# Kernel tuning notes

Measured on AMD Instinct MI355X. Metric: run time of the kernel, lower is better.

Reference implementation:

```python
import jax, jax.numpy as jnp
import numpy as np

N_NODES = 100000   # total nodes in batched graph
N_EDGES = 800000   # total edges
N_GRAPH = 64       # graphs in batch
N_PASSES = 3


def _mlp(x, w1, b1, w2, b2, w3, b3):
    h = jax.nn.relu(x @ w1 + b1)
    h = jax.nn.relu(h @ w2 + b2)
    return h @ w3 + b3


def _segment_mean(x, ids, num_segments):
    # tf.math.unsorted_segment_mean: empty segments -> 0
    s = jax.ops.segment_sum(x, ids, num_segments=num_segments)
    c = jax.ops.segment_sum(jnp.ones((x.shape[0], 1), x.dtype), ids, num_segments=num_segments)
    return s / jnp.maximum(c, 1.0)


def setup_inputs() -> dict:
    key = jax.random.key(0)
    ks = jax.random.split(key, 16)
    nodes = jax.random.normal(ks[0], (N_NODES, 32), jnp.float32)
    edges = jax.random.normal(ks[1], (N_EDGES, 32), jnp.float32)
    globals_ = jax.random.normal(ks[2], (N_GRAPH, 16), jnp.float32)
    senders = jax.random.randint(ks[3], (N_EDGES,), 0, N_NODES, jnp.int32)
    receivers = jax.random.randint(ks[4], (N_EDGES,), 0, N_NODES, jnp.int32)
    node_gid = jnp.sort(jax.random.randint(ks[5], (N_NODES,), 0, N_GRAPH, jnp.int32))
    edge_gid = jnp.sort(jax.random.randint(ks[6], (N_EDGES,), 0, N_GRAPH, jnp.int32))

    def dense(k, din, dout):
        kw, _ = jax.random.split(k)
        w = jax.random.normal(kw, (din, dout), jnp.float32) / np.sqrt(din).astype(np.float32)
        b = jnp.zeros((dout,), jnp.float32)
        return w, b

    e_w1, e_b1 = dense(ks[7], 112, 16)
    e_w2, e_b2 = dense(ks[8], 16, 16)
    e_w3, e_b3 = dense(ks[9], 16, 32)
    n_w1, n_b1 = dense(ks[10], 80, 16)
    n_w2, n_b2 = dense(ks[11], 16, 16)
    n_w3, n_b3 = dense(ks[12], 16, 32)
    g_w1, g_b1 = dense(ks[13], 80, 16)
    g_w2, g_b2 = dense(ks[14], 16, 16)
    g_w3, g_b3 = dense(ks[15], 16, 16)
    return dict(nodes=nodes, edges=edges, globals_=globals_, senders=senders,
                receivers=receivers, node_gid=node_gid, edge_gid=edge_gid,
                e_w1=e_w1, e_b1=e_b1, e_w2=e_w2, e_b2=e_b2, e_w3=e_w3, e_b3=e_b3,
                n_w1=n_w1, n_b1=n_b1, n_w2=n_w2, n_b2=n_b2, n_w3=n_w3, n_b3=n_b3,
                g_w1=g_w1, g_b1=g_b1, g_w2=g_w2, g_b2=g_b2, g_w3=g_w3, g_b3=g_b3)


def reference(nodes, edges, globals_, senders, receivers, node_gid, edge_gid,
              e_w1, e_b1, e_w2, e_b2, e_w3, e_b3,
              n_w1, n_b1, n_w2, n_b2, n_w3, n_b3,
              g_w1, g_b1, g_w2, g_b2, g_w3, g_b3):
    for _ in range(N_PASSES):
        # Edge block: [edges, receiver nodes, sender nodes, broadcast globals]
        e_in = jnp.concatenate([edges, nodes[receivers], nodes[senders], globals_[edge_gid]], axis=-1)
        edges = _mlp(e_in, e_w1, e_b1, e_w2, e_b2, e_w3, e_b3)
        # Node block: [mean of received edges, nodes, broadcast globals]
        agg_e = _segment_mean(edges, receivers, N_NODES)
        n_in = jnp.concatenate([agg_e, nodes, globals_[node_gid]], axis=-1)
        nodes = _mlp(n_in, n_w1, n_b1, n_w2, n_b2, n_w3, n_b3)
        # Global block: [mean edges per graph, mean nodes per graph, globals]
        g_in = jnp.concatenate([_segment_mean(edges, edge_gid, N_GRAPH),
                                _segment_mean(nodes, node_gid, N_GRAPH),
                                globals_], axis=-1)
        globals_ = _mlp(g_in, g_w1, g_b1, g_w2, g_b2, g_w3, g_b3)
    return nodes, edges, globals_
```

## Files before the change

### kernel.cpp

```cpp
#include <hip/hip_runtime.h>
#include <hip/hip_fp16.h>

#define DEV_INLINE __device__ __forceinline__

static const int SCAN_B = 512;

DEV_INLINE int lower_bound_i(const int* __restrict__ a, int n, int v) {
    int lo = 0, hi = n;
    while (lo < hi) { int m = (lo + hi) >> 1; if (a[m] < v) lo = m + 1; else hi = m; }
    return lo;
}

DEV_INLINE void fma4a(float (&h)[16], const float* __restrict__ W,
                      float a0, float a1, float a2, float a3) {
#pragma unroll
    for (int j = 0; j < 16; j++) h[j] = fmaf(a0, W[0 * 16 + j], h[j]);
#pragma unroll
    for (int j = 0; j < 16; j++) h[j] = fmaf(a1, W[1 * 16 + j], h[j]);
#pragma unroll
    for (int j = 0; j < 16; j++) h[j] = fmaf(a2, W[2 * 16 + j], h[j]);
#pragma unroll
    for (int j = 0; j < 16; j++) h[j] = fmaf(a3, W[3 * 16 + j], h[j]);
}
DEV_INLINE void fma4(float (&h)[16], const float* __restrict__ W, float4 a) {
    fma4a(h, W, a.x, a.y, a.z, a.w);
}

DEV_INLINE unsigned f2h2(float a, float b) {
    __half2 h = __floats2half2_rn(a, b);
    return *reinterpret_cast<unsigned*>(&h);
}
DEV_INLINE float2 h2f2(unsigned u) {
    __half2 h;
    *reinterpret_cast<unsigned*>(&h) = u;
    return __half22float2(h);
}
DEV_INLINE void unpack8(uint4 u, float* f) {
    float2 a = h2f2(u.x), b = h2f2(u.y), c = h2f2(u.z), d = h2f2(u.w);
    f[0]=a.x; f[1]=a.y; f[2]=b.x; f[3]=b.y; f[4]=c.x; f[5]=c.y; f[6]=d.x; f[7]=d.y;
}
DEV_INLINE uint4 pack8(const float* f) {
    return make_uint4(f2h2(f[0],f[1]), f2h2(f[2],f[3]), f2h2(f[4],f[5]), f2h2(f[6],f[7]));
}

__global__ void hist_kernel(const int* __restrict__ receivers, int n_edges,
                            int* __restrict__ cnt) {
    int i = blockIdx.x * blockDim.x + threadIdx.x;
    if (i < n_edges) atomicAdd(&cnt[receivers[i]], 1);
}

__global__ __launch_bounds__(SCAN_B)
void scan_block_kernel(const int* __restrict__ cnt, int n,
                       int* __restrict__ scan_tmp, int* __restrict__ blk_sum) {
    __shared__ int s[SCAN_B];
    int tid = threadIdx.x;
    int i = blockIdx.x * SCAN_B + tid;
    int v = (i < n) ? cnt[i] : 0;
    s[tid] = v;
    __syncthreads();
    for (int off = 1; off < SCAN_B; off <<= 1) {
        int t = (tid >= off) ? s[tid - off] : 0;
        __syncthreads();
        s[tid] += t;
        __syncthreads();
    }
    if (i < n) scan_tmp[i] = s[tid];
    if (tid == SCAN_B - 1) blk_sum[blockIdx.x] = s[tid];
}

__global__ __launch_bounds__(1024)
void scan_top_kernel(int* __restrict__ blk_sum, int nb, int* __restrict__ blk_off) {
    __shared__ int s[1024];
    int tid = threadIdx.x;
    int v = (tid < nb) ? blk_sum[tid] : 0;
    s[tid] = v;
    __syncthreads();
    for (int off = 1; off < 1024; off <<= 1) {
        int t = (tid >= off) ? s[tid - off] : 0;
        __syncthreads();
        s[tid] += t;
        __syncthreads();
    }
    if (tid < nb) blk_off[tid] = s[tid] - v;
}

__global__ __launch_bounds__(SCAN_B)
void scan_finalize_kernel(const int* __restrict__ cnt, const int* __restrict__ scan_tmp,
                          const int* __restrict__ blk_off, int n,
                          int* __restrict__ row_ptr, int* __restrict__ running) {
    int i = blockIdx.x * SCAN_B + threadIdx.x;
    if (i >= n) return;
    int incl = scan_tmp[i] + blk_off[i / SCAN_B];
    row_ptr[i + 1] = incl;
    running[i] = incl - cnt[i];
    if (i == 0) row_ptr[0] = 0;
}

__global__ void fill_kernel(const int* __restrict__ receivers, int n_edges,
                            int* __restrict__ running, int* __restrict__ col_idx) {
    int e = blockIdx.x * blockDim.x + threadIdx.x;
    if (e >= n_edges) return;
    int pos = atomicAdd(&running[receivers[e]], 1);
    col_idx[pos] = e;
}

__global__ __launch_bounds__(256)
void node_proj_kernel(const float* __restrict__ nodes_in,
                      const float* __restrict__ glob_prev,
                      float* __restrict__ glob_cur,
                      float* __restrict__ gsum_e, float* __restrict__ gsum_n,
                      const int* __restrict__ edge_gid, int n_edges,
                      const int* __restrict__ node_gid, int n_nodes,
                      const float* __restrict__ gW1, const float* __restrict__ gB1,
                      const float* __restrict__ gW2, const float* __restrict__ gB2,
                      const float* __restrict__ gW3, const float* __restrict__ gB3,
                      const float* __restrict__ eW1, const float* __restrict__ eB1,
                      const float* __restrict__ nW1, const float* __restrict__ nB1,
                      __half* __restrict__ proj,
                      float* __restrict__ biasE, float* __restrict__ biasN,
                      int n_graph) {
    const int n0 = blockIdx.x * 256 + threadIdx.x;
    const int n  = min(n0, n_nodes - 1);
    const float4* pn = (const float4*)nodes_in + (size_t)n * 8;
    float4 xn[8];
#pragma unroll
    for (int q = 0; q < 8; q++) xn[q] = pn[q];

    float hr[16], hs[16];
#pragma unroll
    for (int j = 0; j < 16; j++) { hr[j] = 0.0f; hs[j] = 0.0f; }
#pragma unroll
    for (int q = 0; q < 8; q++) fma4(hr, eW1 + (32 + q * 4) * 16, xn[q]);
#pragma unroll
    for (int q = 0; q < 8; q++) fma4(hs, eW1 + (64 + q * 4) * 16, xn[q]);

    if (n0 < n_nodes) {
        uint4* po = (uint4*)(proj + (size_t)n0 * 32);
        po[0] = pack8(hr);
        po[1] = pack8(hr + 8);
        po[2] = pack8(hs);
        po[3] = pack8(hs + 8);
    }

    if (blockIdx.x == 0) {
        const int g = threadIdx.x;
        float gval[16];
        if (g < n_graph) {
            if (glob_cur) {
                int ecnt = lower_bound_i(edge_gid, n_edges, g + 1) - lower_bound_i(edge_gid, n_edges, g);
                int ncnt = lower_bound_i(node_gid, n_nodes, g + 1) - lower_bound_i(node_gid, n_nodes, g);
                float inv_e = 1.0f / fmaxf((float)ecnt, 1.0f);
                float inv_n = 1.0f / fmaxf((float)ncnt, 1.0f);
                float h1[16];
#pragma unroll
                for (int j = 0; j < 16; j++) h1[j] = gB1[j];
                float x[32];
#pragma unroll
                for (int q = 0; q < 8; q++) {
                    float4 v = ((const float4*)gsum_e)[(size_t)g * 8 + q];
                    x[q*4+0]=v.x*inv_e; x[q*4+1]=v.y*inv_e; x[q*4+2]=v.z*inv_e; x[q*4+3]=v.w*inv_e;
                }
#pragma unroll
                for (int k = 0; k < 32; k++)
#pragma unroll
                    for (int j = 0; j < 16; j++) h1[j] = fmaf(x[k], gW1[k * 16 + j], h1[j]);
#pragma unroll
                for (int q = 0; q < 8; q++) {
                    float4 v = ((const float4*)gsum_n)[(size_t)g * 8 + q];
                    x[q*4+0]=v.x*inv_n; x[q*4+1]=v.y*inv_n; x[q*4+2]=v.z*inv_n; x[q*4+3]=v.w*inv_n;
                }
#pragma unroll
                for (int k = 0; k < 32; k++)
#pragma unroll
                    for (int j = 0; j < 16; j++) h1[j] = fmaf(x[k], gW1[(32 + k) * 16 + j], h1[j]);
                float xg[16];
#pragma unroll
                for (int q = 0; q < 4; q++) {
                    float4 v = ((const float4*)glob_prev)[(size_t)g * 4 + q];
                    xg[q*4+0]=v.x; xg[q*4+1]=v.y; xg[q*4+2]=v.z; xg[q*4+3]=v.w;
                }
#pragma unroll
                for (int k = 0; k < 16; k++)
#pragma unroll
                    for (int j = 0; j < 16; j++) h1[j] = fmaf(xg[k], gW1[(64 + k) * 16 + j], h1[j]);
                float x2[16];
#pragma unroll
                for (int j = 0; j < 16; j++) x2[j] = fmaxf(h1[j], 0.0f);
                float h2[16];
#pragma unroll
                for (int j = 0; j < 16; j++) h2[j] = gB2[j];
#pragma unroll
                for (int k = 0; k < 16; k++)
#pragma unroll
                    for (int j = 0; j < 16; j++) h2[j] = fmaf(x2[k], gW2[k * 16 + j], h2[j]);
                float x3[16];
#pragma unroll
                for (int j = 0; j < 16; j++) x3[j] = fmaxf(h2[j], 0.0f);
#pragma unroll
                for (int j = 0; j < 16; j++) gval[j] = gB3[j];
#pragma unroll
                for (int k = 0; k < 16; k++)
#pragma unroll
                    for (int j = 0; j < 16; j++) gval[j] = fmaf(x3[k], gW3[k * 16 + j], gval[j]);
#pragma unroll
                for (int j = 0; j < 16; j++) glob_cur[g * 16 + j] = gval[j];
            } else {
#pragma unroll
                for (int j = 0; j < 16; j++) gval[j] = glob_prev[g * 16 + j];
            }
        }
        __syncthreads();
        for (int i = threadIdx.x; i < n_graph * 32; i += 256) {
            gsum_e[i] = 0.0f;
            gsum_n[i] = 0.0f;
        }
        if (g < n_graph) {
            float he[16], hn[16];
#pragma unroll
            for (int j = 0; j < 16; j++) { he[j] = eB1[j]; hn[j] = nB1[j]; }
#pragma unroll
            for (int k = 0; k < 16; k++)
#pragma unroll
                for (int j = 0; j < 16; j++) he[j] = fmaf(gval[k], eW1[(96 + k) * 16 + j], he[j]);
#pragma unroll
            for (int k = 0; k < 16; k++)
#pragma unroll
                for (int j = 0; j < 16; j++) hn[j] = fmaf(gval[k], nW1[(64 + k) * 16 + j], hn[j]);
#pragma unroll
            for (int j = 0; j < 16; j++) biasE[g * 16 + j] = he[j];
#pragma unroll
            for (int j = 0; j < 16; j++) biasN[g * 16 + j] = hn[j];
        }
    }
}

template<bool INH, bool OUTH>
__global__ __launch_bounds__(256)
void edge_block_kernel(const void* __restrict__ edges_in_v,
                       const __half* __restrict__ proj,
                       const float* __restrict__ biasE,
                       const int* __restrict__ senders,
                       const int* __restrict__ receivers,
                       const int* __restrict__ edge_gid,
                       const float* __restrict__ W1,
                       const float* __restrict__ W2, const float* __restrict__ B2,
                       const float* __restrict__ W3, const float* __restrict__ B3,
                       void* __restrict__ edges_out_v,
                       int n_edges) {
    const int e0 = blockIdx.x * 256 + threadIdx.x;
    const int e  = min(e0, n_edges - 1);

    const int rr = receivers[e], ss = senders[e], gg = edge_gid[e];

    float xe[32];
    if (INH) {
        const uint4* pe = (const uint4*)((const __half*)edges_in_v + (size_t)e * 32);
        uint4 u0 = pe[0], u1 = pe[1], u2 = pe[2], u3 = pe[3];
        unpack8(u0, xe); unpack8(u1, xe + 8); unpack8(u2, xe + 16); unpack8(u3, xe + 24);
    } else {
        const float4* pe = (const float4*)edges_in_v + (size_t)e * 8;
#pragma unroll
        for (int q = 0; q < 8; q++) {
            float4 v = pe[q];
            xe[q*4+0]=v.x; xe[q*4+1]=v.y; xe[q*4+2]=v.z; xe[q*4+3]=v.w;
        }
    }

    const uint4*  pr = (const uint4*)(proj + (size_t)rr * 32);
    const uint4*  ps = (const uint4*)(proj + (size_t)ss * 32 + 16);
    const float4* pb = (const float4*)biasE + (size_t)gg * 4;

    uint4 r0 = pr[0], r1 = pr[1];
    uint4 s0 = ps[0], s1 = ps[1];
    float4 xb[4];
#pragma unroll
    for (int q = 0; q < 4; q++) xb[q] = pb[q];

    float r[16], s[16];
    unpack8(r0, r); unpack8(r1, r + 8);
    unpack8(s0, s); unpack8(s1, s + 8);

    float h1[16];
#pragma unroll
    for (int q = 0; q < 4; q++) {
        h1[q*4+0] = xb[q].x + r[q*4+0] + s[q*4+0];
        h1[q*4+1] = xb[q].y + r[q*4+1] + s[q*4+1];
        h1[q*4+2] = xb[q].z + r[q*4+2] + s[q*4+2];
        h1[q*4+3] = xb[q].w + r[q*4+3] + s[q*4+3];
    }
#pragma unroll
    for (int q = 0; q < 8; q++)
        fma4a(h1, W1 + (q * 4) * 16, xe[q*4+0], xe[q*4+1], xe[q*4+2], xe[q*4+3]);

    float x2[16];
#pragma unroll
    for (int j = 0; j < 16; j++) x2[j] = fmaxf(h1[j], 0.0f);
    float h2[16];
#pragma unroll
    for (int j = 0; j < 16; j++) h2[j] = B2[j];
#pragma unroll
    for (int k = 0; k < 16; k++)
#pragma unroll
        for (int j = 0; j < 16; j++) h2[j] = fmaf(x2[k], W2[k * 16 + j], h2[j]);

    float x3[16];
#pragma unroll
    for (int j = 0; j < 16; j++) x3[j] = fmaxf(h2[j], 0.0f);
    float o[32];
#pragma unroll
    for (int j = 0; j < 32; j++) o[j] = B3[j];
#pragma unroll
    for (int k = 0; k < 16; k++)
#pragma unroll
        for (int j = 0; j < 32; j++)
            o[j] = fmaf(x3[k], W3[k * 32 + j], o[j]);

    if (e0 < n_edges) {
        if (OUTH) {
            uint4* eo = (uint4*)((__half*)edges_out_v + (size_t)e0 * 32);
            eo[0] = pack8(o); eo[1] = pack8(o + 8); eo[2] = pack8(o + 16); eo[3] = pack8(o + 24);
        } else {
            float4* eo = (float4*)edges_out_v + (size_t)e0 * 8;
#pragma unroll
            for (int j4 = 0; j4 < 8; j4++)
                eo[j4] = make_float4(o[j4*4+0], o[j4*4+1], o[j4*4+2], o[j4*4+3]);
        }
    }
}

template<bool INH>
__global__ __launch_bounds__(256)
void agg_mean_kernel(const void* __restrict__ edges_data_v,
                     const int* __restrict__ col_idx,
                     const int* __restrict__ row_ptr,
                     float* __restrict__ agg_mean, int n_nodes) {
    int node = blockIdx.x * 32 + (threadIdx.x >> 3);
    int lane = threadIdx.x & 7;
    if (node >= n_nodes) return;
    int lo = row_ptr[node], hi = row_ptr[node + 1];
    float4 acc = make_float4(0.f, 0.f, 0.f, 0.f);
    for (int e = lo; e < hi; e++) {
        int idx = col_idx[e];
        if (INH) {
            const uint2* p = (const uint2*)((const __half*)edges_data_v + (size_t)idx * 32 + lane * 4);
            uint2 u = *p;
            float2 a = h2f2(u.x), b = h2f2(u.y);
            acc.x += a.x; acc.y += a.y; acc.z += b.x; acc.w += b.y;
        } else {
            float4 v = ((const float4*)((const float*)edges_data_v + (size_t)idx * 32))[lane];
            acc.x += v.x; acc.y += v.y; acc.z += v.z; acc.w += v.w;
        }
    }
    float inv = 1.0f / fmaxf((float)(hi - lo), 1.0f);
    ((float4*)(agg_mean + (size_t)node * 32))[lane] =
        make_float4(acc.x * inv, acc.y * inv, acc.z * inv, acc.w * inv);
}

__global__ __launch_bounds__(256)
void node_block_kernel(const float* __restrict__ agg_mean,
                       const float* __restrict__ nodes_in,
                       const float* __restrict__ biasN,
                       const int* __restrict__ node_gid,
                       const float* __restrict__ W1,
                       const float* __restrict__ W2, const float* __restrict__ B2,
                       const float* __restrict__ W3, const float* __restrict__ B3,
                       float* __restrict__ nodes_out,
                       int n_nodes) {
    const int n0 = blockIdx.x * 256 + threadIdx.x;
    const int n  = min(n0, n_nodes - 1);
    const int gg = node_gid[n];

    const float4* pa = (const float4*)agg_mean + (size_t)n * 8;
    const float4* pn = (const float4*)nodes_in + (size_t)n * 8;
    const float4* pb = (const float4*)biasN + (size_t)gg * 4;

    float4 xa[8], xn[8], xb[4];
#pragma unroll
    for (int q = 0; q < 8; q++) xa[q] = pa[q];
#pragma unroll
    for (int q = 0; q < 8; q++) xn[q] = pn[q];
#pragma unroll
    for (int q = 0; q < 4; q++) xb[q] = pb[q];

    float h1[16];
#pragma unroll
    for (int q = 0; q < 4; q++) {
        h1[q*4+0] = xb[q].x; h1[q*4+1] = xb[q].y; h1[q*4+2] = xb[q].z; h1[q*4+3] = xb[q].w;
    }
#pragma unroll
    for (int q = 0; q < 8; q++) fma4(h1, W1 + (q * 4) * 16, xa[q]);
#pragma unroll
    for (int q = 0; q < 8; q++) fma4(h1, W1 + (32 + q * 4) * 16, xn[q]);

    float x2[16];
#pragma unroll
    for (int j = 0; j < 16; j++) x2[j] = fmaxf(h1[j], 0.0f);
    float h2[16];
#pragma unroll
    for (int j = 0; j < 16; j++) h2[j] = B2[j];
#pragma unroll
    for (int k = 0; k < 16; k++)
#pragma unroll
        for (int j = 0; j < 16; j++) h2[j] = fmaf(x2[k], W2[k * 16 + j], h2[j]);

    float x3[16];
#pragma unroll
    for (int j = 0; j < 16; j++) x3[j] = fmaxf(h2[j], 0.0f);
    float o[32];
#pragma unroll
    for (int j = 0; j < 32; j++) o[j] = B3[j];
#pragma unroll
    for (int k = 0; k < 16; k++)
#pragma unroll
        for (int j = 0; j < 32; j++)
            o[j] = fmaf(x3[k], W3[k * 32 + j], o[j]);

    if (n0 < n_nodes) {
        float4* no = (float4*)(nodes_out + (size_t)n0 * 32);
#pragma unroll
        for (int j4 = 0; j4 < 8; j4++)
            no[j4] = make_float4(o[j4*4+0], o[j4*4+1], o[j4*4+2], o[j4*4+3]);
    }
}

template<bool INH>
__global__ __launch_bounds__(256)
void graph_sum_kernel(const void* __restrict__ x_v, const int* __restrict__ gid,
                      int n_rows, float* __restrict__ sums, int splits) {
    int g = blockIdx.x / splits;
    int s = blockIdx.x % splits;
    int lo = lower_bound_i(gid, n_rows, g);
    int hi = lower_bound_i(gid, n_rows, g + 1);
    int len = hi - lo;
    int chunk = (len + splits - 1) / splits;
    int rlo = lo + s * chunk;
    int rhi = min(rlo + chunk, hi);

    int c = threadIdx.x & 31;
    int rg = threadIdx.x >> 5;
    float acc = 0.0f;
    for (int r = rlo + rg; r < rhi; r += 8) {
        if (INH) acc += __half2float(((const __half*)x_v)[(size_t)r * 32 + c]);
        else     acc += ((const float*)x_v)[(size_t)r * 32 + c];
    }

    __shared__ float red[256];
    red[threadIdx.x] = acc;
    __syncthreads();
    if (threadIdx.x < 32) {
        float ssum = 0.0f;
#pragma unroll
        for (int i = 0; i < 8; i++) ssum += red[i * 32 + threadIdx.x];
        atomicAdd(&sums[g * 32 + threadIdx.x], ssum);
    }
}

__global__ __launch_bounds__(64)
void global_block_kernel(const float* __restrict__ gsum_e,
                         const float* __restrict__ gsum_n,
                         const float* __restrict__ glob_in,
                         const int* __restrict__ edge_gid, int n_edges,
                         const int* __restrict__ node_gid, int n_nodes,
                         const float* __restrict__ W1, const float* __restrict__ B1,
                         const float* __restrict__ W2, const float* __restrict__ B2,
                         const float* __restrict__ W3, const float* __restrict__ B3,
                         float* __restrict__ glob_out, int n_graph) {
    const int g0 = threadIdx.x;
    const int g  = min(g0, n_graph - 1);

    int ecnt = lower_bound_i(edge_gid, n_edges, g + 1) - lower_bound_i(edge_gid, n_edges, g);
    int ncnt = lower_bound_i(node_gid, n_nodes, g + 1) - lower_bound_i(node_gid, n_nodes, g);
    float inv_e = 1.0f / fmaxf((float)ecnt, 1.0f);
    float inv_n = 1.0f / fmaxf((float)ncnt, 1.0f);

    float h1[16];
#pragma unroll
    for (int j = 0; j < 16; j++) h1[j] = B1[j];

    {
        float x[32];
#pragma unroll
        for (int q = 0; q < 8; q++) {
            float4 v = ((const float4*)gsum_e)[(size_t)g * 8 + q];
            x[q*4+0]=v.x*inv_e; x[q*4+1]=v.y*inv_e; x[q*4+2]=v.z*inv_e; x[q*4+3]=v.w*inv_e;
        }
#pragma unroll
        for (int k = 0; k < 32; k++)
#pragma unroll
            for (int j = 0; j < 16; j++) h1[j] = fmaf(x[k], W1[k * 16 + j], h1[j]);
#pragma unroll
        for (int q = 0; q < 8; q++) {
            float4 v = ((const float4*)gsum_n)[(size_t)g * 8 + q];
            x[q*4+0]=v.x*inv_n; x[q*4+1]=v.y*inv_n; x[q*4+2]=v.z*inv_n; x[q*4+3]=v.w*inv_n;
        }
#pragma unroll
        for (int k = 0; k < 32; k++)
#pragma unroll
            for (int j = 0; j < 16; j++) h1[j] = fmaf(x[k], W1[(32 + k) * 16 + j], h1[j]);
    }
    {
        float xg[16];
#pragma unroll
        for (int q = 0; q < 4; q++) {
            float4 v = ((const float4*)glob_in)[(size_t)g * 4 + q];
            xg[q*4+0]=v.x; xg[q*4+1]=v.y; xg[q*4+2]=v.z; xg[q*4+3]=v.w;
        }
#pragma unroll
        for (int k = 0; k < 16; k++)
#pragma unroll
            for (int j = 0; j < 16; j++) h1[j] = fmaf(xg[k], W1[(64 + k) * 16 + j], h1[j]);
    }

    float x2[16];
#pragma unroll
    for (int j = 0; j < 16; j++) x2[j] = fmaxf(h1[j], 0.0f);
    float h2[16];
#pragma unroll
    for (int j = 0; j < 16; j++) h2[j] = B2[j];
#pragma unroll
    for (int k = 0; k < 16; k++)
#pragma unroll
        for (int j = 0; j < 16; j++) h2[j] = fmaf(x2[k], W2[k * 16 + j], h2[j]);

    float x3[16];
#pragma unroll
    for (int j = 0; j < 16; j++) x3[j] = fmaxf(h2[j], 0.0f);
    float o[16];
#pragma unroll
    for (int j = 0; j < 16; j++) o[j] = B3[j];
#pragma unroll
    for (int k = 0; k < 16; k++)
#pragma unroll
        for (int j = 0; j < 16; j++) o[j] = fmaf(x3[k], W3[k * 16 + j], o[j]);

    if (g0 < n_graph) {
#pragma unroll
        for (int j = 0; j < 16; j++) glob_out[g0 * 16 + j] = o[j];
    }
}

extern "C" void kernel_launch(void* const* d_in, const int* in_sizes, int n_in,
                              void* d_out, int out_size, void* d_ws, size_t ws_size,
                              hipStream_t stream) {
    const float* d_nodes = (const float*)d_in[0];
    const float* d_edges = (const float*)d_in[1];
    const float* d_glob  = (const float*)d_in[2];
    const int* senders   = (const int*)d_in[3];
    const int* receivers = (const int*)d_in[4];
    const int* node_gid  = (const int*)d_in[5];
    const int* edge_gid  = (const int*)d_in[6];
    const float* e_w1 = (const float*)d_in[7];
    const float* e_b1 = (const float*)d_in[8];
    const float* e_w2 = (const float*)d_in[9];
    const float* e_b2 = (const float*)d_in[10];
    const float* e_w3 = (const float*)d_in[11];
    const float* e_b3 = (const float*)d_in[12];
    const float* n_w1 = (const float*)d_in[13];
    const float* n_b1 = (const float*)d_in[14];
    const float* n_w2 = (const float*)d_in[15];
    const float* n_b2 = (const float*)d_in[16];
    const float* n_w3 = (const float*)d_in[17];
    const float* n_b3 = (const float*)d_in[18];
    const float* g_w1 = (const float*)d_in[19];
    const float* g_b1 = (const float*)d_in[20];
    const float* g_w2 = (const float*)d_in[21];
    const float* g_b2 = (const float*)d_in[22];
    const float* g_w3 = (const float*)d_in[23];
    const float* g_b3 = (const float*)d_in[24];

    const int n_nodes = in_sizes[0] / 32;
    const int n_edges = in_sizes[1] / 32;
    const int n_graph = in_sizes[2] / 16;

    float* out_nodes = (float*)d_out;
    float* out_edges = out_nodes + (size_t)n_nodes * 32;
    float* out_glob  = out_edges + (size_t)n_edges * 32;

    float* ws = (float*)d_ws;
    float* ws_edges = ws;  ws += (size_t)n_edges * 32;
    float* ws_nodes = ws;  ws += (size_t)n_nodes * 32;
    float* nscratch = ws;  ws += (size_t)n_nodes * 32;
    float* gA       = ws;  ws += (size_t)n_graph * 16;
    float* gB       = ws;  ws += (size_t)n_graph * 16;
    float* gsum_e   = ws;  ws += (size_t)n_graph * 32;
    float* gsum_n   = ws;  ws += (size_t)n_graph * 32;
    float* biasE    = ws;  ws += (size_t)n_graph * 16;
    float* biasN    = ws;  ws += (size_t)n_graph * 16;

    __half* eh0 = (__half*)ws_edges;
    __half* eh1 = eh0 + (size_t)n_edges * 32;

    int* wi = (int*)ws;
    int* cnt      = wi;  wi += n_nodes;
    int* row_ptr  = wi;  wi += n_nodes + 1;
    int* running  = wi;  wi += n_nodes;
    int* scan_tmp = wi;  wi += n_nodes;
    int* col_idx  = wi;  wi += n_edges;
    int* blk_sum  = wi;  wi += 1024;
    int* blk_off  = wi;  wi += 1024;

    const int nblocks_scan = (n_nodes + SCAN_B - 1) / SCAN_B;

    hipMemsetAsync(cnt, 0, (size_t)n_nodes * sizeof(int), stream);
    hist_kernel<<<(n_edges + 255) / 256, 256, 0, stream>>>(receivers, n_edges, cnt);
    scan_block_kernel<<<nblocks_scan, SCAN_B, 0, stream>>>(cnt, n_nodes, scan_tmp, blk_sum);
    scan_top_kernel<<<1, 1024, 0, stream>>>(blk_sum, nblocks_scan, blk_off);
    scan_finalize_kernel<<<nblocks_scan, SCAN_B, 0, stream>>>(cnt, scan_tmp, blk_off,
                                                              n_nodes, row_ptr, running);
    fill_kernel<<<(n_edges + 255) / 256, 256, 0, stream>>>(receivers, n_edges, running, col_idx);

    const float* nodes_in = d_nodes;
    const float* glob_states[4] = { d_glob, gA, gB, out_glob };
    const int eb_grid = (n_edges + 255) / 256;
    const int nb_grid = (n_nodes + 255) / 256;

    for (int pass = 0; pass < 3; ++pass) {
        float* nodes_out = (pass == 1) ? ws_nodes : out_nodes;

        node_proj_kernel<<<nb_grid, 256, 0, stream>>>(
            nodes_in,
            glob_states[pass == 0 ? 0 : pass - 1],
            pass == 0 ? nullptr : (float*)glob_states[pass],
            gsum_e, gsum_n,
            edge_gid, n_edges, node_gid, n_nodes,
            g_w1, g_b1, g_w2, g_b2, g_w3, g_b3,
            e_w1, e_b1, n_w1, n_b1,
            (__half*)nscratch, biasE, biasN, n_graph);

        if (pass == 0) {
            edge_block_kernel<false, true><<<eb_grid, 256, 0, stream>>>(
                d_edges, (const __half*)nscratch, biasE, senders, receivers, edge_gid,
                e_w1, e_w2, e_b2, e_w3, e_b3, eh0, n_edges);
            graph_sum_kernel<true><<<n_graph * 16, 256, 0, stream>>>(eh0, edge_gid, n_edges, gsum_e, 16);
            agg_mean_kernel<true><<<(n_nodes + 31) / 32, 256, 0, stream>>>(
                eh0, col_idx, row_ptr, nscratch, n_nodes);
        } else if (pass == 1) {
            edge_block_kernel<true, true><<<eb_grid, 256, 0, stream>>>(
                eh0, (const __half*)nscratch, biasE, senders, receivers, edge_gid,
                e_w1, e_w2, e_b2, e_w3, e_b3, eh1, n_edges);
            graph_sum_kernel<true><<<n_graph * 16, 256, 0, stream>>>(eh1, edge_gid, n_edges, gsum_e, 16);
            agg_mean_kernel<true><<<(n_nodes + 31) / 32, 256, 0, stream>>>(
                eh1, col_idx, row_ptr, nscratch, n_nodes);
        } else {
            edge_block_kernel<true, false><<<eb_grid, 256, 0, stream>>>(
                eh1, (const __half*)nscratch, biasE, senders, receivers, edge_gid,
                e_w1, e_w2, e_b2, e_w3, e_b3, out_edges, n_edges);
            graph_sum_kernel<false><<<n_graph * 16, 256, 0, stream>>>(out_edges, edge_gid, n_edges, gsum_e, 16);
            agg_mean_kernel<false><<<(n_nodes + 31) / 32, 256, 0, stream>>>(
                out_edges, col_idx, row_ptr, nscratch, n_nodes);
        }

        node_block_kernel<<<nb_grid, 256, 0, stream>>>(
            nscratch, nodes_in, biasN, node_gid,
            n_w1, n_w2, n_b2, n_w3, n_b3,
            nodes_out, n_nodes);

        graph_sum_kernel<false><<<n_graph * 4, 256, 0, stream>>>(nodes_out, node_gid, n_nodes, gsum_n, 4);

        nodes_in = nodes_out;
    }

    global_block_kernel<<<1, 64, 0, stream>>>(
        gsum_e, gsum_n, gB, edge_gid, n_edges, node_gid, n_nodes,
        g_w1, g_b1, g_w2, g_b2, g_w3, g_b3,
        out_glob, n_graph);
}
```

Measured before the change: 776.8 us.

## Merge edge graph-sum and receiver aggregation into one launch; use nontemporal loads/stores

Combines the per-graph edge sum and the CSR receiver mean aggregation into a single kernel, with block ranges split between the two tasks, so one launch replaces two per pass. Adds nontemporal load/store builtins to the edge block and the consume kernel for streaming edge data, indices and outputs. The aim is to cut launch overhead and let the two reductions run concurrently. Nontemporal hints could hurt reuse, since the edge outputs are re-read right away by the next kernel and would otherwise hit in cache.

After: 975.0 us. +25.5%, slower.

```diff
diff --git a/kernel.cpp b/kernel.cpp
--- a/kernel.cpp
+++ b/kernel.cpp
@@ -4,6 +4,34 @@
 #define DEV_INLINE __device__ __forceinline__
 
 static const int SCAN_B = 512;
+
+typedef unsigned uvec4 __attribute__((ext_vector_type(4)));
+typedef unsigned uvec2 __attribute__((ext_vector_type(2)));
+typedef float    fvec4 __attribute__((ext_vector_type(4)));
+
+DEV_INLINE int   ntload_i(const int* p)  { return __builtin_nontemporal_load(p); }
+DEV_INLINE uint4 ntload_u4(const uint4* p) {
+    uvec4 v = __builtin_nontemporal_load((const uvec4*)p);
+    return make_uint4(v.x, v.y, v.z, v.w);
+}
+DEV_INLINE uint2 ntload_u2(const uint2* p) {
+    uvec2 v = __builtin_nontemporal_load((const uvec2*)p);
+    return make_uint2(v.x, v.y);
+}
+DEV_INLINE float4 ntload_f4(const float4* p) {
+    fvec4 v = __builtin_nontemporal_load((const fvec4*)p);
+    return make_float4(v.x, v.y, v.z, v.w);
+}
+DEV_INLINE float ntload_f(const float* p) { return __builtin_nontemporal_load(p); }
+DEV_INLINE unsigned short ntload_h(const unsigned short* p) { return __builtin_nontemporal_load(p); }
+DEV_INLINE void ntstore_u4(uint4* p, uint4 v) {
+    uvec4 t; t.x = v.x; t.y = v.y; t.z = v.z; t.w = v.w;
+    __builtin_nontemporal_store(t, (uvec4*)p);
+}
+DEV_INLINE void ntstore_f4(float4* p, float4 v) {
+    fvec4 t; t.x = v.x; t.y = v.y; t.z = v.z; t.w = v.w;
+    __builtin_nontemporal_store(t, (fvec4*)p);
+}
 
 DEV_INLINE int lower_bound_i(const int* __restrict__ a, int n, int v) {
     int lo = 0, hi = n;
@@ -250,18 +278,21 @@
     const int e0 = blockIdx.x * 256 + threadIdx.x;
     const int e  = min(e0, n_edges - 1);
 
-    const int rr = receivers[e], ss = senders[e], gg = edge_gid[e];
+    const int rr = ntload_i(receivers + e);
+    const int ss = ntload_i(senders + e);
+    const int gg = ntload_i(edge_gid + e);
 
     float xe[32];
     if (INH) {
         const uint4* pe = (const uint4*)((const __half*)edges_in_v + (size_t)e * 32);
-        uint4 u0 = pe[0], u1 = pe[1], u2 = pe[2], u3 = pe[3];
+        uint4 u0 = ntload_u4(pe + 0), u1 = ntload_u4(pe + 1);
+        uint4 u2 = ntload_u4(pe + 2), u3 = ntload_u4(pe + 3);
         unpack8(u0, xe); unpack8(u1, xe + 8); unpack8(u2, xe + 16); unpack8(u3, xe + 24);
     } else {
         const float4* pe = (const float4*)edges_in_v + (size_t)e * 8;
 #pragma unroll
         for (int q = 0; q < 8; q++) {
-            float4 v = pe[q];
+            float4 v = ntload_f4(pe + q);
             xe[q*4+0]=v.x; xe[q*4+1]=v.y; xe[q*4+2]=v.z; xe[q*4+3]=v.w;
         }
     }
@@ -318,42 +349,82 @@
     if (e0 < n_edges) {
         if (OUTH) {
             uint4* eo = (uint4*)((__half*)edges_out_v + (size_t)e0 * 32);
-            eo[0] = pack8(o); eo[1] = pack8(o + 8); eo[2] = pack8(o + 16); eo[3] = pack8(o + 24);
+            ntstore_u4(eo + 0, pack8(o));
+            ntstore_u4(eo + 1, pack8(o + 8));
+            ntstore_u4(eo + 2, pack8(o + 16));
+            ntstore_u4(eo + 3, pack8(o + 24));
         } else {
             float4* eo = (float4*)edges_out_v + (size_t)e0 * 8;
 #pragma unroll
             for (int j4 = 0; j4 < 8; j4++)
-                eo[j4] = make_float4(o[j4*4+0], o[j4*4+1], o[j4*4+2], o[j4*4+3]);
+                ntstore_f4(eo + j4, make_float4(o[j4*4+0], o[j4*4+1], o[j4*4+2], o[j4*4+3]));
         }
     }
 }
 
 template<bool INH>
 __global__ __launch_bounds__(256)
-void agg_mean_kernel(const void* __restrict__ edges_data_v,
-                     const int* __restrict__ col_idx,
-                     const int* __restrict__ row_ptr,
-                     float* __restrict__ agg_mean, int n_nodes) {
-    int node = blockIdx.x * 32 + (threadIdx.x >> 3);
-    int lane = threadIdx.x & 7;
-    if (node >= n_nodes) return;
-    int lo = row_ptr[node], hi = row_ptr[node + 1];
-    float4 acc = make_float4(0.f, 0.f, 0.f, 0.f);
-    for (int e = lo; e < hi; e++) {
-        int idx = col_idx[e];
-        if (INH) {
-            const uint2* p = (const uint2*)((const __half*)edges_data_v + (size_t)idx * 32 + lane * 4);
-            uint2 u = *p;
-            float2 a = h2f2(u.x), b = h2f2(u.y);
-            acc.x += a.x; acc.y += a.y; acc.z += b.x; acc.w += b.y;
-        } else {
-            float4 v = ((const float4*)((const float*)edges_data_v + (size_t)idx * 32))[lane];
-            acc.x += v.x; acc.y += v.y; acc.z += v.z; acc.w += v.w;
-        }
-    }
-    float inv = 1.0f / fmaxf((float)(hi - lo), 1.0f);
-    ((float4*)(agg_mean + (size_t)node * 32))[lane] =
-        make_float4(acc.x * inv, acc.y * inv, acc.z * inv, acc.w * inv);
+void edge_consume_kernel(const void* __restrict__ edges_data_v,
+                         const int* __restrict__ gid, int n_edges,
+                         float* __restrict__ gsum,
+                         const int* __restrict__ col_idx,
+                         const int* __restrict__ row_ptr,
+                         float* __restrict__ agg_mean, int n_nodes, int n_graph) {
+    __shared__ float red[256];
+    const int GS_BLOCKS = n_graph * 16;
+
+    if ((int)blockIdx.x < GS_BLOCKS) {
+        int g = blockIdx.x >> 4;
+        int s = blockIdx.x & 15;
+        int lo = lower_bound_i(gid, n_edges, g);
+        int hi = lower_bound_i(gid, n_edges, g + 1);
+        int len = hi - lo;
+        int chunk = (len + 15) / 16;
+        int rlo = lo + s * chunk;
+        int rhi = min(rlo + chunk, hi);
+
+        int c = threadIdx.x & 31;
+        int rg = threadIdx.x >> 5;
+        float acc = 0.0f;
+        for (int r = rlo + rg; r < rhi; r += 8) {
+            if (INH) {
+                unsigned short u = ntload_h((const unsigned short*)edges_data_v + (size_t)r * 32 + c);
+                __half hh; *reinterpret_cast<unsigned short*>(&hh) = u;
+                acc += __half2float(hh);
+            } else {
+                acc += ntload_f((const float*)edges_data_v + (size_t)r * 32 + c);
+            }
+        }
+        red[threadIdx.x] = acc;
+        __syncthreads();
+        if (threadIdx.x < 32) {
+            float ssum = 0.0f;
+#pragma unroll
+            for (int i = 0; i < 8; i++) ssum += red[i * 32 + threadIdx.x];
+            atomicAdd(&gsum[g * 32 + threadIdx.x], ssum);
+        }
+    } else {
+        int bb = blockIdx.x - GS_BLOCKS;
+        int node = bb * 32 + (threadIdx.x >> 3);
+        int lane = threadIdx.x & 7;
+        if (node >= n_nodes) return;
+        int lo = row_ptr[node], hi = row_ptr[node + 1];
+        float4 acc = make_float4(0.f, 0.f, 0.f, 0.f);
+        for (int e = lo; e < hi; e++) {
+            int idx = ntload_i(col_idx + e);
+            if (INH) {
+                uint2 u = ntload_u2((const uint2*)((const __half*)edges_data_v + (size_t)idx * 32 + lane * 4));
+                float2 a = h2f2(u.x), b = h2f2(u.y);
+                acc.x += a.x; acc.y += a.y; acc.z += b.x; acc.w += b.y;
+            } else {
+                float4 v = ntload_f4((const float4*)((const float*)edges_data_v + (size_t)idx * 32) + lane);
+                acc.x += v.x; acc.y += v.y; acc.z += v.z; acc.w += v.w;
+            }
+        }
+        float inv = 1.0f / fmaxf((float)(hi - lo), 1.0f);
+        ((float4*)(agg_mean + (size_t)node * 32))[lane] =
+            make_float4(acc.x * inv, acc.y * inv, acc.z * inv, acc.w * inv);
+    }
 }
 
 __global__ __launch_bounds__(256)
@@ -423,9 +494,8 @@
     }
 }
 
-template<bool INH>
 __global__ __launch_bounds__(256)
-void graph_sum_kernel(const void* __restrict__ x_v, const int* __restrict__ gid,
+void graph_sum_kernel(const float* __restrict__ x, const int* __restrict__ gid,
                       int n_rows, float* __restrict__ sums, int splits) {
     int g = blockIdx.x / splits;
     int s = blockIdx.x % splits;
@@ -439,10 +509,8 @@
     int c = threadIdx.x & 31;
     int rg = threadIdx.x >> 5;
     float acc = 0.0f;
-    for (int r = rlo + rg; r < rhi; r += 8) {
-        if (INH) acc += __half2float(((const __half*)x_v)[(size_t)r * 32 + c]);
-        else     acc += ((const float*)x_v)[(size_t)r * 32 + c];
-    }
+    for (int r = rlo + rg; r < rhi; r += 8)
+        acc += x[(size_t)r * 32 + c];
 
     __shared__ float red[256];
     red[threadIdx.x] = acc;
@@ -613,6 +681,7 @@
     const float* glob_states[4] = { d_glob, gA, gB, out_glob };
     const int eb_grid = (n_edges + 255) / 256;
     const int nb_grid = (n_nodes + 255) / 256;
+    const int consume_grid = n_graph * 16 + (n_nodes + 31) / 32;
 
     for (int pass = 0; pass < 3; ++pass) {
         float* nodes_out = (pass == 1) ? ws_nodes : out_nodes;
@@ -631,23 +700,20 @@
             edge_block_kernel<false, true><<<eb_grid, 256, 0, stream>>>(
                 d_edges, (const __half*)nscratch, biasE, senders, receivers, edge_gid,
                 e_w1, e_w2, e_b2, e_w3, e_b3, eh0, n_edges);
-            graph_sum_kernel<true><<<n_graph * 16, 256, 0, stream>>>(eh0, edge_gid, n_edges, gsum_e, 16);
-            agg_mean_kernel<true><<<(n_nodes + 31) / 32, 256, 0, stream>>>(
-                eh0, col_idx, row_ptr, nscratch, n_nodes);
+            edge_consume_kernel<true><<<consume_grid, 256, 0, stream>>>(
+                eh0, edge_gid, n_edges, gsum_e, col_idx, row_ptr, nscratch, n_nodes, n_graph);
         } else if (pass == 1) {
             edge_block_kernel<true, true><<<eb_grid, 256, 0, stream>>>(
                 eh0, (const __half*)nscratch, biasE, senders, receivers, edge_gid,
                 e_w1, e_w2, e_b2, e_w3, e_b3, eh1, n_edges);
-            graph_sum_kernel<true><<<n_graph * 16, 256, 0, stream>>>(eh1, edge_gid, n_edges, gsum_e, 16);
-            agg_mean_kernel<true><<<(n_nodes + 31) / 32, 256, 0, stream>>>(
-                eh1, col_idx, row_ptr, nscratch, n_nodes);
+            edge_consume_kernel<true><<<consume_grid, 256, 0, stream>>>(
+                eh1, edge_gid, n_edges, gsum_e, col_idx, row_ptr, nscratch, n_nodes, n_graph);
         } else {
             edge_block_kernel<true, false><<<eb_grid, 256, 0, stream>>>(
                 eh1, (const __half*)nscratch, biasE, senders, receivers, edge_gid,
                 e_w1, e_w2, e_b2, e_w3, e_b3, out_edges, n_edges);
-            graph_sum_kernel<false><<<n_graph * 16, 256, 0, stream>>>(out_edges, edge_gid, n_edges, gsum_e, 16);
-            agg_mean_kernel<false><<<(n_nodes + 31) / 32, 256, 0, stream>>>(
-                out_edges, col_idx, row_ptr, nscratch, n_nodes);
+            edge_consume_kernel<false><<<consume_grid, 256, 0, stream>>>(
+                out_edges, edge_gid, n_edges, gsum_e, col_idx, row_ptr, nscratch, n_nodes, n_graph);
         }
 
         node_block_kernel<<<nb_grid, 256, 0, stream>>>(
@@ -655,7 +721,7 @@
             n_w1, n_w2, n_b2, n_w3, n_b3,
             nodes_out, n_nodes);
 
-        graph_sum_kernel<false><<<n_graph * 4, 256, 0, stream>>>(nodes_out, node_gid, n_nodes, gsum_n, 4);
+        graph_sum_kernel<<<n_graph * 4, 256, 0, stream>>>(nodes_out, node_gid, n_nodes, gsum_n, 4);
 
         nodes_in = nodes_out;
     }
```
